# Kernel optimization log

Measured on AMD Instinct MI355X. Metric: run time of the kernel, lower is better.

Reference implementation:

```python
import jax, jax.numpy as jnp
import numpy as np

H = 128   # image height
W = 128   # image width
K = 8     # points_per_pixel


def setup_inputs() -> dict:
    key = jax.random.key(0)
    k1, k2 = jax.random.split(key)
    P = 8192
    # xy in NDC [-1, 1], z in front of the camera (z >= 0 per the kernel's pz < 0 skip)
    xy = jax.random.uniform(k1, (P, 2), minval=-1.0, maxval=1.0, dtype=jnp.float32)
    z = jax.random.uniform(k2, (P, 1), minval=0.05, maxval=1.0, dtype=jnp.float32)
    points = jnp.concatenate([xy, z], axis=-1)           # (P, 3)
    radius = jnp.full((P,), 0.03, dtype=jnp.float32)     # per-point NDC radius
    return {"points": points, "radius": radius}


def reference(points, radius):
    """Dense z-buffer point rasterization (PyTorch3D rasterize_points semantics, N=1).

    Returns (idx, zbuf, dists2), each of shape (1, H, W, K); slots hit by fewer
    than K points are padded with -1.
    """
    P = points.shape[0]
    x, y, z = points[:, 0], points[:, 1], points[:, 2]

    # Pixel centers in NDC: xf = PixToNdc(W-1-xi, W) = 1 - (2*xi+1)/W (x right-to-left),
    # yf = PixToNdc(H-1-yi, H) = 1 - (2*yi+1)/H (y bottom-to-top).
    xf = 1.0 - (2.0 * jnp.arange(W, dtype=points.dtype) + 1.0) / W   # (W,)
    yf = 1.0 - (2.0 * jnp.arange(H, dtype=points.dtype) + 1.0) / H   # (H,)

    dx = xf[None, :, None] - x[None, None, :]   # (1, W, P) -> (H, W, P)
    dy = yf[:, None, None] - y[None, None, :]   # (H, 1, P) -> (H, W, P)
    dist2 = dx * dx + dy * dy                   # (H, W, P) squared xy distance

    inside = dist2 < (radius * radius)[None, None, :]
    valid = inside & (z >= 0.0)[None, None, :]  # kernel skips points behind camera

    # k smallest z among valid candidates per pixel
    score = jnp.where(valid, z[None, None, :], jnp.inf)   # (H, W, P)
    _, idx = jax.lax.top_k(-score, K)                     # (H, W, K)

    zk = z[idx]                                  # (H, W, K)
    dk = jnp.take_along_axis(dist2, idx, axis=-1)
    vk = jnp.take_along_axis(valid, idx, axis=-1)

    idx_out = jnp.where(vk, idx, -1).astype(jnp.int32)[None]   # (1, H, W, K)
    zbuf = jnp.where(vk, zk, -1.0)[None]
    dists = jnp.where(vk, dk, -1.0)[None]
    return idx_out, zbuf, dists
```

## Files before the change

kernel.cpp:

```cpp
#include <hip/hip_runtime.h>

#define HH 128
#define WW 128
#define KK 8
#define TILE 8
#define TX (WW / TILE)
#define TY (HH / TILE)
#define NTILES (TX * TY)
#define NWAVES 4
#define CAP 1024
#define IMAX 0x7fffffff

__device__ __forceinline__ float bcastf(float v, int lane) {
    return __int_as_float(__builtin_amdgcn_readlane(__float_as_int(v), lane));
}
__device__ __forceinline__ int bcasti(int v, int lane) {
    return __builtin_amdgcn_readlane(v, lane);
}

#define CSTEP(zh, ih, dh, zl, il, dl)                                 \
    {                                                                 \
        bool sw_ = (zh < zl) || (zh == zl && ih < il);                \
        float tz_ = sw_ ? zl : zh; int ti_ = sw_ ? il : ih;           \
        float td_ = sw_ ? dl : dh;                                    \
        zl = sw_ ? zh : zl; il = sw_ ? ih : il; dl = sw_ ? dh : dl;   \
        zh = tz_; ih = ti_; dh = td_;                                 \
    }

#define INSERT(z, p, dd)                                              \
    {                                                                 \
        z7 = z; i7 = p; d7 = dd;                                      \
        CSTEP(z7, i7, d7, z6, i6, d6);                                \
        CSTEP(z6, i6, d6, z5, i5, d5);                                \
        CSTEP(z5, i5, d5, z4, i4, d4);                                \
        CSTEP(z4, i4, d4, z3, i3, d3);                                \
        CSTEP(z3, i3, d3, z2, i2, d2s);                               \
        CSTEP(z2, i2, d2s, z1, i1, d1);                               \
        CSTEP(z1, i1, d1, z0, i0, d0);                                \
    }

__global__ void __launch_bounds__(256) fused_raster_kernel(
                              const float* __restrict__ pts,
                              const float* __restrict__ rad,
                              int P,
                              float* __restrict__ out) {
    int t = blockIdx.x;
    int th = t / TX, tw = t % TX;
    int tid = threadIdx.x;
    int wv = tid >> 6;
    int lane = tid & 63;
    int pw = lane % TILE, ph = lane / TILE;
    int w = tw * TILE + pw;
    int h = th * TILE + ph;

    __shared__ float4 scand[CAP];
    __shared__ int    sidx[CAP];
    __shared__ int    scnt;
    __shared__ float lz[NWAVES - 1][KK][64];
    __shared__ int   li[NWAVES - 1][KK][64];
    __shared__ float ld[NWAVES - 1][KK][64];

    if (tid == 0) scnt = 0;
    __syncthreads();

    for (int p = tid; p < P; p += 256) {
        float x = pts[3 * p + 0];
        float y = pts[3 * p + 1];
        float z = pts[3 * p + 2];
        float r = rad[p];
        if (!(z >= 0.0f) || !(r > 0.0f)) continue;

        float wlo = (WW * (1.0f - x - r) - 1.0f) * 0.5f;
        float whi = (WW * (1.0f - x + r) - 1.0f) * 0.5f;
        int wmin = max(0, (int)ceilf(wlo - 0.05f));
        int wmax = min(WW - 1, (int)floorf(whi + 0.05f));
        float hlo = (HH * (1.0f - y - r) - 1.0f) * 0.5f;
        float hhi = (HH * (1.0f - y + r) - 1.0f) * 0.5f;
        int hmin = max(0, (int)ceilf(hlo - 0.05f));
        int hmax = min(HH - 1, (int)floorf(hhi + 0.05f));
        if (wmin > wmax || hmin > hmax) continue;
        if (tw < wmin / TILE || tw > wmax / TILE) continue;
        if (th < hmin / TILE || th > hmax / TILE) continue;

        int slot = atomicAdd(&scnt, 1);
        if (slot < CAP) {
            scand[slot] = make_float4(x, y, z, __fmul_rn(r, r));
            sidx[slot] = p;
        }
    }
    __syncthreads();
    int cnt = min(scnt, CAP);

    float z0 = INFINITY, z1 = INFINITY, z2 = INFINITY, z3 = INFINITY,
          z4 = INFINITY, z5 = INFINITY, z6 = INFINITY, z7 = INFINITY;
    int   i0 = IMAX, i1 = IMAX, i2 = IMAX, i3 = IMAX,
          i4 = IMAX, i5 = IMAX, i6 = IMAX, i7 = IMAX;
    float d0 = -1.f, d1 = -1.f, d2s = -1.f, d3 = -1.f,
          d4 = -1.f, d5 = -1.f, d6 = -1.f, d7 = -1.f;

    float xf = 1.0f - (2.0f * (float)w + 1.0f) * (1.0f / (float)WW);
    float yf = 1.0f - (2.0f * (float)h + 1.0f) * (1.0f / (float)HH);

    int S = (cnt + NWAVES - 1) / NWAVES;
    int s0 = wv * S;
    int s1 = min(cnt, s0 + S);

    for (int base = s0; base < s1; base += 64) {
        int n = min(64, s1 - base);
        float4 cur = make_float4(0.f, 0.f, 0.f, 0.f);
        int cpi = 0;
        if (base + lane < s1) { cur = scand[base + lane]; cpi = sidx[base + lane]; }

        for (int j = 0; j < n; ++j) {
            float x  = bcastf(cur.x, j);
            float y  = bcastf(cur.y, j);
            float z  = bcastf(cur.z, j);
            float r2 = bcastf(cur.w, j);
            int   p  = bcasti(cpi, j);
            float dx = xf - x;
            float dy = yf - y;
            float dd = __fadd_rn(__fmul_rn(dx, dx), __fmul_rn(dy, dy));
            if (dd < r2 && ((z < z7) || (z == z7 && p < i7))) {
                INSERT(z, p, dd);
            }
        }
    }

    if (wv > 0) {
        int m = wv - 1;
        lz[m][0][lane] = z0; li[m][0][lane] = i0; ld[m][0][lane] = d0;
        lz[m][1][lane] = z1; li[m][1][lane] = i1; ld[m][1][lane] = d1;
        lz[m][2][lane] = z2; li[m][2][lane] = i2; ld[m][2][lane] = d2s;
        lz[m][3][lane] = z3; li[m][3][lane] = i3; ld[m][3][lane] = d3;
        lz[m][4][lane] = z4; li[m][4][lane] = i4; ld[m][4][lane] = d4;
        lz[m][5][lane] = z5; li[m][5][lane] = i5; ld[m][5][lane] = d5;
        lz[m][6][lane] = z6; li[m][6][lane] = i6; ld[m][6][lane] = d6;
        lz[m][7][lane] = z7; li[m][7][lane] = i7; ld[m][7][lane] = d7;
    }
    __syncthreads();
    if (wv != 0) return;

#pragma unroll
    for (int m = 0; m < NWAVES - 1; ++m) {
        for (int k = 0; k < KK; ++k) {
            float z = lz[m][k][lane];
            int   p = li[m][k][lane];
            float dd = ld[m][k][lane];
            bool ins = (z < z7) || (z == z7 && p < i7);
            if (!__builtin_amdgcn_ballot_w64(ins)) break;
            if (ins) INSERT(z, p, dd);
        }
    }

    int pix = h * WW + w;
    float* o_idx = out;
    float* o_z   = out + HH * WW * KK;
    float* o_d   = out + 2 * HH * WW * KK;

    bool v0 = i0 != IMAX, v1 = i1 != IMAX, v2 = i2 != IMAX, v3 = i3 != IMAX;
    bool v4 = i4 != IMAX, v5 = i5 != IMAX, v6 = i6 != IMAX, v7 = i7 != IMAX;

    float4 fi_lo = make_float4(v0 ? (float)i0 : -1.f, v1 ? (float)i1 : -1.f,
                               v2 ? (float)i2 : -1.f, v3 ? (float)i3 : -1.f);
    float4 fi_hi = make_float4(v4 ? (float)i4 : -1.f, v5 ? (float)i5 : -1.f,
                               v6 ? (float)i6 : -1.f, v7 ? (float)i7 : -1.f);
    float4 fz_lo = make_float4(v0 ? z0 : -1.f, v1 ? z1 : -1.f,
                               v2 ? z2 : -1.f, v3 ? z3 : -1.f);
    float4 fz_hi = make_float4(v4 ? z4 : -1.f, v5 ? z5 : -1.f,
                               v6 ? z6 : -1.f, v7 ? z7 : -1.f);
    float4 fd_lo = make_float4(v0 ? d0 : -1.f, v1 ? d1 : -1.f,
                               v2 ? d2s : -1.f, v3 ? d3 : -1.f);
    float4 fd_hi = make_float4(v4 ? d4 : -1.f, v5 ? d5 : -1.f,
                               v6 ? d6 : -1.f, v7 ? d7 : -1.f);

    float4* oi = (float4*)(o_idx + pix * KK);
    float4* oz = (float4*)(o_z   + pix * KK);
    float4* od = (float4*)(o_d   + pix * KK);
    oi[0] = fi_lo; oi[1] = fi_hi;
    oz[0] = fz_lo; oz[1] = fz_hi;
    od[0] = fd_lo; od[1] = fd_hi;
}

extern "C" void kernel_launch(void* const* d_in, const int* in_sizes, int n_in,
                              void* d_out, int out_size, void* d_ws, size_t ws_size,
                              hipStream_t stream) {
    const float* pts = (const float*)d_in[0];
    const float* rad = (const float*)d_in[1];
    int P = in_sizes[0] / 3;

    fused_raster_kernel<<<NTILES, 256, 0, stream>>>(pts, rad, P, (float*)d_out);
}
```

Before: 31.96 us.

## Use 512-thread blocks, unroll point binning 4x with simpler tile-bounds test

Doubles the block to 8 waves, so each tile's candidate list is split across more waves and the cross-wave merge grows to seven partial lists. The binning loop now loads four points per thread per iteration for memory-level parallelism. It replaces the per-point pixel-range ceil/floor computation with a direct NDC bounding-box test against the tile's pixel-center extents plus a small epsilon. The bigger merge and the larger shared-memory footprint (and thus fewer resident blocks) are the costs, and the epsilon test may admit slightly different candidates at the edges, though the exact distance test still decides the result.

```diff
diff --git a/kernel.cpp b/kernel.cpp
--- a/kernel.cpp
+++ b/kernel.cpp
@@ -7,9 +7,11 @@
 #define TX (WW / TILE)
 #define TY (HH / TILE)
 #define NTILES (TX * TY)
-#define NWAVES 4
+#define NW 8
+#define NT 512
 #define CAP 1024
 #define IMAX 0x7fffffff
+#define EPS 1e-3f
 
 __device__ __forceinline__ float bcastf(float v, int lane) {
     return __int_as_float(__builtin_amdgcn_readlane(__float_as_int(v), lane));
@@ -39,7 +41,7 @@
         CSTEP(z1, i1, d1, z0, i0, d0);                                \
     }
 
-__global__ void __launch_bounds__(256) fused_raster_kernel(
+__global__ void __launch_bounds__(NT) fused_raster_kernel(
                               const float* __restrict__ pts,
                               const float* __restrict__ rad,
                               int P,
@@ -56,37 +58,47 @@
     __shared__ float4 scand[CAP];
     __shared__ int    sidx[CAP];
     __shared__ int    scnt;
-    __shared__ float lz[NWAVES - 1][KK][64];
-    __shared__ int   li[NWAVES - 1][KK][64];
-    __shared__ float ld[NWAVES - 1][KK][64];
+    __shared__ float lz[NW - 1][KK][64];
+    __shared__ int   li[NW - 1][KK][64];
+    __shared__ float ld[NW - 1][KK][64];
 
     if (tid == 0) scnt = 0;
     __syncthreads();
 
-    for (int p = tid; p < P; p += 256) {
-        float x = pts[3 * p + 0];
-        float y = pts[3 * p + 1];
-        float z = pts[3 * p + 2];
-        float r = rad[p];
-        if (!(z >= 0.0f) || !(r > 0.0f)) continue;
-
-        float wlo = (WW * (1.0f - x - r) - 1.0f) * 0.5f;
-        float whi = (WW * (1.0f - x + r) - 1.0f) * 0.5f;
-        int wmin = max(0, (int)ceilf(wlo - 0.05f));
-        int wmax = min(WW - 1, (int)floorf(whi + 0.05f));
-        float hlo = (HH * (1.0f - y - r) - 1.0f) * 0.5f;
-        float hhi = (HH * (1.0f - y + r) - 1.0f) * 0.5f;
-        int hmin = max(0, (int)ceilf(hlo - 0.05f));
-        int hmax = min(HH - 1, (int)floorf(hhi + 0.05f));
-        if (wmin > wmax || hmin > hmax) continue;
-        if (tw < wmin / TILE || tw > wmax / TILE) continue;
-        if (th < hmin / TILE || th > hmax / TILE) continue;
-
-        int slot = atomicAdd(&scnt, 1);
-        if (slot < CAP) {
-            scand[slot] = make_float4(x, y, z, __fmul_rn(r, r));
-            sidx[slot] = p;
+    float xhi_c = 1.0f - (2.0f * (float)(tw * TILE) + 1.0f) * (1.0f / WW);
+    float xlo_c = 1.0f - (2.0f * (float)(tw * TILE + TILE - 1) + 1.0f) * (1.0f / WW);
+    float yhi_c = 1.0f - (2.0f * (float)(th * TILE) + 1.0f) * (1.0f / HH);
+    float ylo_c = 1.0f - (2.0f * (float)(th * TILE + TILE - 1) + 1.0f) * (1.0f / HH);
+
+    for (int base = 0; base < P; base += NT * 4) {
+        int p0 = base + tid;
+        int p1 = p0 + NT, p2 = p0 + 2 * NT, p3 = p0 + 3 * NT;
+        bool g0 = p0 < P, g1 = p1 < P, g2 = p2 < P, g3 = p3 < P;
+        float x0 = g0 ? pts[3 * p0] : 2.f, y0 = g0 ? pts[3 * p0 + 1] : 2.f,
+              zz0 = g0 ? pts[3 * p0 + 2] : -1.f, r0 = g0 ? rad[p0] : 0.f;
+        float x1 = g1 ? pts[3 * p1] : 2.f, y1 = g1 ? pts[3 * p1 + 1] : 2.f,
+              zz1 = g1 ? pts[3 * p1 + 2] : -1.f, r1 = g1 ? rad[p1] : 0.f;
+        float x2 = g2 ? pts[3 * p2] : 2.f, y2 = g2 ? pts[3 * p2 + 1] : 2.f,
+              zz2 = g2 ? pts[3 * p2 + 2] : -1.f, r2v = g2 ? rad[p2] : 0.f;
+        float x3 = g3 ? pts[3 * p3] : 2.f, y3 = g3 ? pts[3 * p3 + 1] : 2.f,
+              zz3 = g3 ? pts[3 * p3 + 2] : -1.f, r3 = g3 ? rad[p3] : 0.f;
+
+#define CONSIDER(p, x, y, z, r)                                           \
+        if ((z >= 0.0f) && (r > 0.0f) &&                                  \
+            (x > xlo_c - r - EPS) && (x < xhi_c + r + EPS) &&             \
+            (y > ylo_c - r - EPS) && (y < yhi_c + r + EPS)) {             \
+            int slot = atomicAdd(&scnt, 1);                               \
+            if (slot < CAP) {                                             \
+                scand[slot] = make_float4(x, y, z, __fmul_rn(r, r));      \
+                sidx[slot] = p;                                           \
+            }                                                             \
         }
+
+        CONSIDER(p0, x0, y0, zz0, r0)
+        CONSIDER(p1, x1, y1, zz1, r1)
+        CONSIDER(p2, x2, y2, zz2, r2v)
+        CONSIDER(p3, x3, y3, zz3, r3)
+#undef CONSIDER
     }
     __syncthreads();
     int cnt = min(scnt, CAP);
@@ -101,7 +113,7 @@
     float xf = 1.0f - (2.0f * (float)w + 1.0f) * (1.0f / (float)WW);
     float yf = 1.0f - (2.0f * (float)h + 1.0f) * (1.0f / (float)HH);
 
-    int S = (cnt + NWAVES - 1) / NWAVES;
+    int S = (cnt + NW - 1) / NW;
     int s0 = wv * S;
     int s1 = min(cnt, s0 + S);
 
@@ -141,7 +153,7 @@
     if (wv != 0) return;
 
 #pragma unroll
-    for (int m = 0; m < NWAVES - 1; ++m) {
+    for (int m = 0; m < NW - 1; ++m) {
         for (int k = 0; k < KK; ++k) {
             float z = lz[m][k][lane];
             int   p = li[m][k][lane];
@@ -187,6 +199,7 @@
     const float* pts = (const float*)d_in[0];
     const float* rad = (const float*)d_in[1];
     int P = in_sizes[0] / 3;
-
-    fused_raster_kernel<<<NTILES, 256, 0, stream>>>(pts, rad, P, (float*)d_out);
-}
+    (void)d_ws; (void)ws_size;
+
+    fused_raster_kernel<<<NTILES, NT, 0, stream>>>(pts, rad, P, (float*)d_out);
+}
```

New measurement: 27.32 us. 1.17x faster.
